# Kernel tuning notes

Measured on AMD Instinct MI355X. Metric: run time of the kernel, lower is better.

## Reference

```python
import jax, jax.numpy as jnp
import numpy as np

N = 50000      # nodes
E = 800000     # edges (avg degree 16)
SIZES = [128, 128, 128, 128, 64]
NUM_LAYERS = 4


def setup_inputs() -> dict:
    key = jax.random.key(0)
    ks = jax.random.split(key, 3 + 2 * NUM_LAYERS)
    inp = {
        "x": jax.random.normal(ks[0], (N, SIZES[0]), dtype=jnp.float32),
        "edge_index": jax.random.randint(ks[1], (2, E), 0, N, dtype=jnp.int64),
        "edge_weight": jax.random.uniform(ks[2], (E,), dtype=jnp.float32),
    }
    for i in range(NUM_LAYERS):
        fan_in = SIZES[i]
        inp[f"W{i}"] = (jax.random.normal(ks[3 + 2 * i], (SIZES[i], SIZES[i + 1]), dtype=jnp.float32)
                        / np.float32(np.sqrt(fan_in)))
        inp[f"b{i}"] = jnp.zeros((SIZES[i + 1],), dtype=jnp.float32)
    return inp


def gcn_conv(x, src, dst, ew, W, b, n):
    """PyG GCNConv with add_self_loops=True, normalize=True (eval mode).
    deg[i] = sum of incoming edge weights at i + 1 (self loop weight 1).
    norm(j->i) = deg[j]^-1/2 * w_ji * deg[i]^-1/2.
    Self loop contributes deg[i]^-1 * (xW)[i].
    """
    xw = x @ W                                                    # [n, out]
    deg = jax.ops.segment_sum(ew, dst, num_segments=n) + 1.0      # [n]
    dinv = jnp.where(deg > 0, jax.lax.rsqrt(deg), 0.0)            # deg^-1/2
    norm = dinv[src] * ew * dinv[dst]                             # [E]
    agg = jax.ops.segment_sum(xw[src] * norm[:, None], dst, num_segments=n)
    return agg + xw * (dinv * dinv)[:, None] + b


def reference(x, edge_index, edge_weight, W0, b0, W1, b1, W2, b2, W3, b3):
    # Dropout p=0.5 is identity in eval mode (training=False).
    src, dst = edge_index[0], edge_index[1]
    Ws = [W0, W1, W2, W3]
    bs = [b0, b1, b2, b3]
    for i in range(NUM_LAYERS):
        x = gcn_conv(x, src, dst, edge_weight, Ws[i], bs[i], N)
        if i < NUM_LAYERS - 1:
            x = jax.nn.relu(x)
    return x
```

## Files before the change

kernel.cpp:

```cpp
#include <hip/hip_runtime.h>
#include <hip/hip_fp16.h>


#define DEG_SCALE 4194304.0f
#define BCAP 5120
#define K1_EDGES 4096

using f16x8 = __attribute__((ext_vector_type(8))) _Float16;
using f32x4 = __attribute__((ext_vector_type(4))) float;

__global__ void prep_kernel(const float* __restrict__ W0, const float* __restrict__ W1,
                            const float* __restrict__ W2, const float* __restrict__ W3,
                            __half* P0, __half* P1, __half* P2, __half* P3,
                            int* gCursor, int nBuckets) {
    int blk = blockIdx.x;
    if (blk == 28) {
        int t = threadIdx.x;
        if (t < nBuckets) gCursor[t] = t * BCAP;
        return;
    }
    int t = blk * 256 + threadIdx.x;
    const float* W;
    __half* P;
    int OUT;
    if (t < 2048)      { W = W0; P = P0; OUT = 128; }
    else if (t < 4096) { W = W1; P = P1; OUT = 128; t -= 2048; }
    else if (t < 6144) { W = W2; P = P2; OUT = 128; t -= 4096; }
    else               { W = W3; P = P3; OUT = 64;  t -= 6144; }
    int lane = t & 63, fi = t >> 6;
    int nt = fi >> 2, kc = fi & 3;
    int col = 16 * nt + (lane & 15);
    int k0  = 32 * kc + 8 * (lane >> 4);
    union { __half h[8]; uint4 u; } v;
#pragma unroll
    for (int j = 0; j < 8; j++) v.h[j] = __float2half_rn(W[(size_t)(k0 + j) * OUT + col]);
    *(uint4*)&P[((size_t)fi * 64 + lane) * 8] = v.u;
}

__global__ __launch_bounds__(256) void bucket_scatter_kernel(
        const int* __restrict__ src, const int* __restrict__ dst,
        const float* __restrict__ ew, int* gCursor,
        int2* __restrict__ bucketArr, int E, int nBuckets) {
    __shared__ int cnt[256];
    __shared__ int runBase[256];
    int tid = threadIdx.x;
    int e0 = blockIdx.x * K1_EDGES;
    int e1 = min(e0 + K1_EDGES, E);
    cnt[tid] = 0;
    __syncthreads();
    for (int e = e0 + tid; e < e1; e += 256)
        atomicAdd(&cnt[dst[e] >> 8], 1);
    __syncthreads();
    if (tid < nBuckets && cnt[tid] > 0)
        runBase[tid] = atomicAdd(&gCursor[tid], cnt[tid]);
    __syncthreads();
    cnt[tid] = 0;
    __syncthreads();
    for (int e = e0 + tid; e < e1; e += 256) {
        int d = dst[e];
        int b = d >> 8;
        int slot = runBase[b] + atomicAdd(&cnt[b], 1);
        if (slot < (b + 1) * BCAP)
            bucketArr[slot] = make_int2((src[e] & 0xFFFF) | (d << 16),
                                        __float_as_int(ew[e]));
    }
}

__global__ __launch_bounds__(256) void bucket_csr_kernel(
        const int2* __restrict__ bucketArr, const int* __restrict__ gCursor,
        int2* __restrict__ epack, int* __restrict__ row_ptr,
        float* __restrict__ dinv, float* __restrict__ dinv2,
        int N, int E, int nBuckets) {
    __shared__ int2 st[BCAP];
    __shared__ int cnt[256];
    __shared__ int scn[256];
    __shared__ int cur[256];
    __shared__ unsigned int dfix[256];
    __shared__ int cbase_sh;
    int b   = blockIdx.x;
    int tid = threadIdx.x;
    int node0 = b << 8;
    int nloc  = min(256, N - node0);
    int base  = b * BCAP;

    int sz = (tid < nBuckets) ? (gCursor[tid] - tid * BCAP) : 0;
    scn[tid] = sz;
    __syncthreads();
    for (int off = 1; off < 256; off <<= 1) {
        int u = (tid >= off) ? scn[tid - off] : 0;
        __syncthreads();
        scn[tid] += u;
        __syncthreads();
    }
    if (tid == b) cbase_sh = scn[tid] - sz;
    cnt[tid]  = 0;
    dfix[tid] = 0u;
    __syncthreads();
    int cbase = cbase_sh;
    int size  = gCursor[b] - base;

    for (int i = tid; i < size; i += 256) {
        int2 v = bucketArr[base + i];
        st[i] = v;
        int dl = (v.x >> 16) & 255;
        atomicAdd(&cnt[dl], 1);
        atomicAdd(&dfix[dl], (unsigned int)rintf(__int_as_float(v.y) * DEG_SCALE));
    }
    __syncthreads();

    if (tid < nloc) {
        float d = (float)dfix[tid] * (1.0f / DEG_SCALE) + 1.0f;
        float r = rsqrtf(d);
        dinv[node0 + tid]  = r;
        dinv2[node0 + tid] = 1.0f / d;
    }

    int val = cnt[tid];
    scn[tid] = val;
    __syncthreads();
    for (int off = 1; off < 256; off <<= 1) {
        int u = (tid >= off) ? scn[tid - off] : 0;
        __syncthreads();
        scn[tid] += u;
        __syncthreads();
    }
    int excl = scn[tid] - val;
    scn[tid] = excl;
    if (tid < nloc) row_ptr[node0 + tid] = cbase + excl;
    if (b == nBuckets - 1 && tid == 0) row_ptr[N] = E;
    cur[tid] = 0;
    __syncthreads();

    for (int i = tid; i < size; i += 256) {
        int2 v = st[i];
        int dl = (v.x >> 16) & 255;
        int p  = cbase + scn[dl] + atomicAdd(&cur[dl], 1);
        epack[p] = v;
    }
}

template <int OUT, bool AFP32>
__device__ __forceinline__ void gemm_body(const void* __restrict__ A,
                                          const __half* __restrict__ Wpack,
                                          __half* __restrict__ xw, int nrows, int bid) {
    constexpr int NT  = OUT / 16;
    constexpr int CPR = OUT / 8;
    __shared__ __half D[64 * OUT];
    int tid  = threadIdx.x;
    int wave = tid >> 6, lane = tid & 63;
    int r = lane & 15, g = lane >> 4;
    int row0 = bid * 64 + wave * 16;

    int arow = row0 + r;
    if (arow >= nrows) arow = nrows - 1;

    f16x8 a[4];
#pragma unroll
    for (int kc = 0; kc < 4; kc++) {
        if (AFP32) {
            const float* p = (const float*)A + (size_t)arow * 128 + kc * 32 + g * 8;
            float4 u = *(const float4*)p;
            float4 v = *(const float4*)(p + 4);
            a[kc][0] = (_Float16)u.x; a[kc][1] = (_Float16)u.y;
            a[kc][2] = (_Float16)u.z; a[kc][3] = (_Float16)u.w;
            a[kc][4] = (_Float16)v.x; a[kc][5] = (_Float16)v.y;
            a[kc][6] = (_Float16)v.z; a[kc][7] = (_Float16)v.w;
        } else {
            a[kc] = *(const f16x8*)((const __half*)A + (size_t)arow * 128 + kc * 32 + g * 8);
        }
    }

#pragma unroll
    for (int nt = 0; nt < NT; nt++) {
        const f16x8* Bp = (const f16x8*)(Wpack) + (size_t)nt * 4 * 64 + lane;
        f32x4 c = {0.f, 0.f, 0.f, 0.f};
        c = __builtin_amdgcn_mfma_f32_16x16x32_f16(a[0], Bp[0],   c, 0, 0, 0);
        c = __builtin_amdgcn_mfma_f32_16x16x32_f16(a[1], Bp[64],  c, 0, 0, 0);
        c = __builtin_amdgcn_mfma_f32_16x16x32_f16(a[2], Bp[128], c, 0, 0, 0);
        c = __builtin_amdgcn_mfma_f32_16x16x32_f16(a[3], Bp[192], c, 0, 0, 0);
        int col = 16 * nt + r;
#pragma unroll
        for (int j = 0; j < 4; j++) {
            int drow = wave * 16 + 4 * g + j;
            int ch   = (col >> 3) ^ (drow & (CPR - 1));
            D[drow * OUT + ch * 8 + (col & 7)] = __float2half_rn(c[j]);
        }
    }
    __syncthreads();
#pragma unroll
    for (int i = 0; i < 64 * CPR / 256; i++) {
        int idx  = tid + i * 256;
        int drow = idx / CPR;
        int ch   = idx % CPR;
        int gr   = bid * 64 + drow;
        if (gr < nrows) {
            f16x8 v = *(f16x8*)&D[drow * OUT + ((ch ^ (drow & (CPR - 1))) << 3)];
            *(f16x8*)&xw[(size_t)gr * OUT + ch * 8] = v;
        }
    }
}

template <int OUT>
__global__ __launch_bounds__(256) void gemm_mfma_kernel(const __half* __restrict__ A,
                                                        const __half* __restrict__ Wpack,
                                                        __half* __restrict__ xw, int nrows) {
    gemm_body<OUT, false>(A, Wpack, xw, nrows, blockIdx.x);
}

__global__ __launch_bounds__(256) void norm_gemm0_kernel(
        int2* __restrict__ epack, const float* __restrict__ dinv, int E, int nbNorm,
        const float* __restrict__ x, const __half* __restrict__ Wpack,
        __half* __restrict__ xw, int nrows) {
    int blk = blockIdx.x;
    if (blk < nbNorm) {
        int i = blk * 256 + threadIdx.x;
        if (i < E) {
            int2 v = epack[i];
            int s = v.x & 0xFFFF;
            int d = (v.x >> 16) & 0xFFFF;
            float nm = dinv[s] * __int_as_float(v.y) * dinv[d];
            epack[i] = make_int2(s, __float_as_int(nm));
        }
        return;
    }
    gemm_body<128, true>(x, Wpack, xw, nrows, blk - nbNorm);
}

__global__ __launch_bounds__(256) void gather128h_kernel(const __half* __restrict__ xwh,
                                                         const int* __restrict__ rp,
                                                         const int2* __restrict__ epack,
                                                         const float* __restrict__ dinv2,
                                                         const float* __restrict__ bias,
                                                         __half* __restrict__ out, int n) {
    int lane = threadIdx.x & 63;
    int node = (blockIdx.x * blockDim.x + threadIdx.x) >> 6;
    if (node >= n) return;
    node = __builtin_amdgcn_readfirstlane(node);
    int e0 = rp[node], e1 = rp[node + 1];
    float ax = 0.f, ay = 0.f;

    int e = e0;
    for (; e + 8 <= e1; e += 8) {
        int2 v0 = epack[e + 0], v1 = epack[e + 1], v2 = epack[e + 2], v3 = epack[e + 3];
        int2 v4 = epack[e + 4], v5 = epack[e + 5], v6 = epack[e + 6], v7 = epack[e + 7];
        __half2 h0 = ((const __half2*)(xwh + (size_t)v0.x * 128))[lane];
        __half2 h1 = ((const __half2*)(xwh + (size_t)v1.x * 128))[lane];
        __half2 h2 = ((const __half2*)(xwh + (size_t)v2.x * 128))[lane];
        __half2 h3 = ((const __half2*)(xwh + (size_t)v3.x * 128))[lane];
        __half2 h4 = ((const __half2*)(xwh + (size_t)v4.x * 128))[lane];
        __half2 h5 = ((const __half2*)(xwh + (size_t)v5.x * 128))[lane];
        __half2 h6 = ((const __half2*)(xwh + (size_t)v6.x * 128))[lane];
        __half2 h7 = ((const __half2*)(xwh + (size_t)v7.x * 128))[lane];
        float w0 = __int_as_float(v0.y), w1 = __int_as_float(v1.y);
        float w2 = __int_as_float(v2.y), w3 = __int_as_float(v3.y);
        float w4 = __int_as_float(v4.y), w5 = __int_as_float(v5.y);
        float w6 = __int_as_float(v6.y), w7 = __int_as_float(v7.y);
        ax += __half2float(h0.x) * w0 + __half2float(h1.x) * w1
            + __half2float(h2.x) * w2 + __half2float(h3.x) * w3
            + __half2float(h4.x) * w4 + __half2float(h5.x) * w5
            + __half2float(h6.x) * w6 + __half2float(h7.x) * w7;
        ay += __half2float(h0.y) * w0 + __half2float(h1.y) * w1
            + __half2float(h2.y) * w2 + __half2float(h3.y) * w3
            + __half2float(h4.y) * w4 + __half2float(h5.y) * w5
            + __half2float(h6.y) * w6 + __half2float(h7.y) * w7;
    }
    for (; e + 2 <= e1; e += 2) {
        int2 v0 = epack[e + 0], v1 = epack[e + 1];
        __half2 h0 = ((const __half2*)(xwh + (size_t)v0.x * 128))[lane];
        __half2 h1 = ((const __half2*)(xwh + (size_t)v1.x * 128))[lane];
        float w0 = __int_as_float(v0.y), w1 = __int_as_float(v1.y);
        ax += __half2float(h0.x) * w0 + __half2float(h1.x) * w1;
        ay += __half2float(h0.y) * w0 + __half2float(h1.y) * w1;
    }
    for (; e < e1; e++) {
        int2 v = epack[e];
        __half2 h = ((const __half2*)(xwh + (size_t)v.x * 128))[lane];
        float w = __int_as_float(v.y);
        ax += __half2float(h.x) * w;
        ay += __half2float(h.y) * w;
    }

    float   d2 = dinv2[node];
    __half2 hs = ((const __half2*)(xwh + (size_t)node * 128))[lane];
    float2  bl = *(const float2*)&bias[lane * 2];
    float ox = fmaxf(ax + __half2float(hs.x) * d2 + bl.x, 0.f);
    float oy = fmaxf(ay + __half2float(hs.y) * d2 + bl.y, 0.f);
    __half2 ho;
    ho.x = __float2half_rn(ox);
    ho.y = __float2half_rn(oy);
    *(__half2*)&out[(size_t)node * 128 + lane * 2] = ho;
}

__global__ __launch_bounds__(256) void gather64h_kernel(const __half* __restrict__ xwh,
                                                        const int* __restrict__ rp,
                                                        const int2* __restrict__ epack,
                                                        const float* __restrict__ dinv2,
                                                        const float* __restrict__ bias,
                                                        float* __restrict__ out, int n) {
    int lane = threadIdx.x & 63;
    int node = (blockIdx.x * blockDim.x + threadIdx.x) >> 6;
    if (node >= n) return;
    node = __builtin_amdgcn_readfirstlane(node);
    int e0 = rp[node], e1 = rp[node + 1];
    float acc = 0.f;

    int e = e0;
    for (; e + 8 <= e1; e += 8) {
        int2 v0 = epack[e + 0], v1 = epack[e + 1], v2 = epack[e + 2], v3 = epack[e + 3];
        int2 v4 = epack[e + 4], v5 = epack[e + 5], v6 = epack[e + 6], v7 = epack[e + 7];
        float r0 = __half2float(xwh[(size_t)v0.x * 64 + lane]);
        float r1 = __half2float(xwh[(size_t)v1.x * 64 + lane]);
        float r2 = __half2float(xwh[(size_t)v2.x * 64 + lane]);
        float r3 = __half2float(xwh[(size_t)v3.x * 64 + lane]);
        float r4 = __half2float(xwh[(size_t)v4.x * 64 + lane]);
        float r5 = __half2float(xwh[(size_t)v5.x * 64 + lane]);
        float r6 = __half2float(xwh[(size_t)v6.x * 64 + lane]);
        float r7 = __half2float(xwh[(size_t)v7.x * 64 + lane]);
        acc += r0 * __int_as_float(v0.y) + r1 * __int_as_float(v1.y)
             + r2 * __int_as_float(v2.y) + r3 * __int_as_float(v3.y)
             + r4 * __int_as_float(v4.y) + r5 * __int_as_float(v5.y)
             + r6 * __int_as_float(v6.y) + r7 * __int_as_float(v7.y);
    }
    for (; e < e1; e++) {
        int2 v = epack[e];
        acc += __half2float(xwh[(size_t)v.x * 64 + lane]) * __int_as_float(v.y);
    }

    float self = __half2float(xwh[(size_t)node * 64 + lane]);
    out[(size_t)node * 64 + lane] = acc + self * dinv2[node] + bias[lane];
}

extern "C" void kernel_launch(void* const* d_in, const int* in_sizes, int n_in,
                              void* d_out, int out_size, void* d_ws, size_t ws_size,
                              hipStream_t stream) {
    const float* x  = (const float*)d_in[0];
    const int*   ei = (const int*)d_in[1];
    const float* ew = (const float*)d_in[2];
    const float* W[4] = {(const float*)d_in[3], (const float*)d_in[5],
                         (const float*)d_in[7], (const float*)d_in[9]};
    const float* b[4] = {(const float*)d_in[4], (const float*)d_in[6],
                         (const float*)d_in[8], (const float*)d_in[10]};
    const int N = in_sizes[0] / 128;
    const int E = in_sizes[2];
    const int* srcIdx = ei;
    const int* dstIdx = ei + E;
    float* out = (float*)d_out;

    const int nBuckets = (N + 255) / 256;

    char* p = (char*)d_ws;
    auto alloc = [&](size_t bytes) -> char* {
        char* q = p;
        p += (bytes + 255) / 256 * 256;
        return q;
    };
    float*  dinv      = (float*)alloc((size_t)N * 4);
    float*  dinv2     = (float*)alloc((size_t)N * 4);
    int*    row_ptr   = (int*)alloc((size_t)(N + 1) * 4);
    int*    gCursor   = (int*)alloc(256 * 4);
    int2*   bucketArr = (int2*)alloc((size_t)nBuckets * BCAP * 8);
    int2*   epack     = (int2*)alloc((size_t)E * 8);
    __half* xwh       = (__half*)alloc((size_t)N * 128 * 2);
    __half* bufA      = (__half*)alloc((size_t)N * 128 * 2);
    __half* Wp[4];
    Wp[0] = (__half*)alloc(128 * 128 * 2);
    Wp[1] = (__half*)alloc(128 * 128 * 2);
    Wp[2] = (__half*)alloc(128 * 128 * 2);
    Wp[3] = (__half*)alloc(128 * 64 * 2);

    const int k1_grid = (E + K1_EDGES - 1) / K1_EDGES;
    const int eb      = (E + 255) / 256;
    const int gemm_grid   = (N + 63) / 64;
    const int gather_grid = (N + 3) / 4;

    prep_kernel<<<29, 256, 0, stream>>>(W[0], W[1], W[2], W[3],
                                        Wp[0], Wp[1], Wp[2], Wp[3],
                                        gCursor, nBuckets);
    bucket_scatter_kernel<<<k1_grid, 256, 0, stream>>>(srcIdx, dstIdx, ew, gCursor,
                                                       bucketArr, E, nBuckets);
    bucket_csr_kernel<<<nBuckets, 256, 0, stream>>>(bucketArr, gCursor, epack,
                                                    row_ptr, dinv, dinv2, N, E, nBuckets);
    norm_gemm0_kernel<<<eb + gemm_grid, 256, 0, stream>>>(epack, dinv, E, eb,
                                                          x, Wp[0], xwh, N);

    const __half* xin;
    for (int i = 0; i < 4; i++) {
        if (i < 3) {
            if (i > 0)
                gemm_mfma_kernel<128><<<gemm_grid, 256, 0, stream>>>(xin, Wp[i], xwh, N);
            gather128h_kernel<<<gather_grid, 256, 0, stream>>>(
                xwh, row_ptr, epack, dinv2, b[i], bufA, N);
            xin = bufA;
        } else {
            gemm_mfma_kernel<64><<<gemm_grid, 256, 0, stream>>>(xin, Wp[3], xwh, N);
            gather64h_kernel<<<gather_grid, 256, 0, stream>>>(
                xwh, row_ptr, epack, dinv2, b[3], out, N);
        }
    }
}
```

Before: 210.5 us.

## Fuse layer gather with next layer's MFMA GEMM in one kernel

Replaces the separate gather128h and gemm_mfma kernels for the hidden layers with one kernel. Each block gathers and aggregates 16 nodes into shared memory, applies bias and ReLU, then multiplies that tile by the next layer's weights with MFMA and writes xW directly. The intent is to remove the round trip of the activation buffer through global memory and three kernel launches. In exchange, each block holds 16 nodes instead of 64, so weights are reloaded more often and the GEMM tile is smaller.

Result: faster. 182.7 us (-13.2%).

```diff
diff --git a/kernel.cpp b/kernel.cpp
--- a/kernel.cpp
+++ b/kernel.cpp
@@ -5,6 +5,7 @@
 #define DEG_SCALE 4194304.0f
 #define BCAP 5120
 #define K1_EDGES 4096
+#define ACT_LD 136
 
 using f16x8 = __attribute__((ext_vector_type(8))) _Float16;
 using f32x4 = __attribute__((ext_vector_type(4))) float;
@@ -200,13 +201,6 @@
     }
 }
 
-template <int OUT>
-__global__ __launch_bounds__(256) void gemm_mfma_kernel(const __half* __restrict__ A,
-                                                        const __half* __restrict__ Wpack,
-                                                        __half* __restrict__ xw, int nrows) {
-    gemm_body<OUT, false>(A, Wpack, xw, nrows, blockIdx.x);
-}
-
 __global__ __launch_bounds__(256) void norm_gemm0_kernel(
         int2* __restrict__ epack, const float* __restrict__ dinv, int E, int nbNorm,
         const float* __restrict__ x, const __half* __restrict__ Wpack,
@@ -226,69 +220,121 @@
     gemm_body<128, true>(x, Wpack, xw, nrows, blk - nbNorm);
 }
 
-__global__ __launch_bounds__(256) void gather128h_kernel(const __half* __restrict__ xwh,
-                                                         const int* __restrict__ rp,
-                                                         const int2* __restrict__ epack,
-                                                         const float* __restrict__ dinv2,
-                                                         const float* __restrict__ bias,
-                                                         __half* __restrict__ out, int n) {
-    int lane = threadIdx.x & 63;
-    int node = (blockIdx.x * blockDim.x + threadIdx.x) >> 6;
-    if (node >= n) return;
-    node = __builtin_amdgcn_readfirstlane(node);
-    int e0 = rp[node], e1 = rp[node + 1];
-    float ax = 0.f, ay = 0.f;
-
-    int e = e0;
-    for (; e + 8 <= e1; e += 8) {
-        int2 v0 = epack[e + 0], v1 = epack[e + 1], v2 = epack[e + 2], v3 = epack[e + 3];
-        int2 v4 = epack[e + 4], v5 = epack[e + 5], v6 = epack[e + 6], v7 = epack[e + 7];
-        __half2 h0 = ((const __half2*)(xwh + (size_t)v0.x * 128))[lane];
-        __half2 h1 = ((const __half2*)(xwh + (size_t)v1.x * 128))[lane];
-        __half2 h2 = ((const __half2*)(xwh + (size_t)v2.x * 128))[lane];
-        __half2 h3 = ((const __half2*)(xwh + (size_t)v3.x * 128))[lane];
-        __half2 h4 = ((const __half2*)(xwh + (size_t)v4.x * 128))[lane];
-        __half2 h5 = ((const __half2*)(xwh + (size_t)v5.x * 128))[lane];
-        __half2 h6 = ((const __half2*)(xwh + (size_t)v6.x * 128))[lane];
-        __half2 h7 = ((const __half2*)(xwh + (size_t)v7.x * 128))[lane];
-        float w0 = __int_as_float(v0.y), w1 = __int_as_float(v1.y);
-        float w2 = __int_as_float(v2.y), w3 = __int_as_float(v3.y);
-        float w4 = __int_as_float(v4.y), w5 = __int_as_float(v5.y);
-        float w6 = __int_as_float(v6.y), w7 = __int_as_float(v7.y);
-        ax += __half2float(h0.x) * w0 + __half2float(h1.x) * w1
-            + __half2float(h2.x) * w2 + __half2float(h3.x) * w3
-            + __half2float(h4.x) * w4 + __half2float(h5.x) * w5
-            + __half2float(h6.x) * w6 + __half2float(h7.x) * w7;
-        ay += __half2float(h0.y) * w0 + __half2float(h1.y) * w1
-            + __half2float(h2.y) * w2 + __half2float(h3.y) * w3
-            + __half2float(h4.y) * w4 + __half2float(h5.y) * w5
-            + __half2float(h6.y) * w6 + __half2float(h7.y) * w7;
-    }
-    for (; e + 2 <= e1; e += 2) {
-        int2 v0 = epack[e + 0], v1 = epack[e + 1];
-        __half2 h0 = ((const __half2*)(xwh + (size_t)v0.x * 128))[lane];
-        __half2 h1 = ((const __half2*)(xwh + (size_t)v1.x * 128))[lane];
-        float w0 = __int_as_float(v0.y), w1 = __int_as_float(v1.y);
-        ax += __half2float(h0.x) * w0 + __half2float(h1.x) * w1;
-        ay += __half2float(h0.y) * w0 + __half2float(h1.y) * w1;
-    }
-    for (; e < e1; e++) {
-        int2 v = epack[e];
-        __half2 h = ((const __half2*)(xwh + (size_t)v.x * 128))[lane];
-        float w = __int_as_float(v.y);
-        ax += __half2float(h.x) * w;
-        ay += __half2float(h.y) * w;
-    }
-
-    float   d2 = dinv2[node];
-    __half2 hs = ((const __half2*)(xwh + (size_t)node * 128))[lane];
-    float2  bl = *(const float2*)&bias[lane * 2];
-    float ox = fmaxf(ax + __half2float(hs.x) * d2 + bl.x, 0.f);
-    float oy = fmaxf(ay + __half2float(hs.y) * d2 + bl.y, 0.f);
-    __half2 ho;
-    ho.x = __float2half_rn(ox);
-    ho.y = __float2half_rn(oy);
-    *(__half2*)&out[(size_t)node * 128 + lane * 2] = ho;
+template <int OUT_NEXT>
+__global__ __launch_bounds__(256) void gather_gemm_kernel(
+        const __half* __restrict__ xwh,
+        const int* __restrict__ rp,
+        const int2* __restrict__ epack,
+        const float* __restrict__ dinv2,
+        const float* __restrict__ bias,
+        const __half* __restrict__ Wpack,
+        __half* __restrict__ xw_out,
+        int n) {
+    constexpr int NT  = OUT_NEXT / 16;
+    constexpr int NTW = NT / 4;
+    constexpr int CPR = OUT_NEXT / 8;
+    __shared__ __half act[16 * ACT_LD];
+    __shared__ __half D[16 * OUT_NEXT];
+    int tid  = threadIdx.x;
+    int wv   = tid >> 6, lane = tid & 63;
+    int node0 = blockIdx.x * 16;
+
+#pragma unroll
+    for (int k = 0; k < 4; k++) {
+        int lrow = wv * 4 + k;
+        int node = node0 + lrow;
+        if (node < n) {
+            node = __builtin_amdgcn_readfirstlane(node);
+            int e0 = rp[node], e1 = rp[node + 1];
+            float ax = 0.f, ay = 0.f;
+            int e = e0;
+            for (; e + 8 <= e1; e += 8) {
+                int2 v0 = epack[e + 0], v1 = epack[e + 1], v2 = epack[e + 2], v3 = epack[e + 3];
+                int2 v4 = epack[e + 4], v5 = epack[e + 5], v6 = epack[e + 6], v7 = epack[e + 7];
+                __half2 h0 = ((const __half2*)(xwh + (size_t)v0.x * 128))[lane];
+                __half2 h1 = ((const __half2*)(xwh + (size_t)v1.x * 128))[lane];
+                __half2 h2 = ((const __half2*)(xwh + (size_t)v2.x * 128))[lane];
+                __half2 h3 = ((const __half2*)(xwh + (size_t)v3.x * 128))[lane];
+                __half2 h4 = ((const __half2*)(xwh + (size_t)v4.x * 128))[lane];
+                __half2 h5 = ((const __half2*)(xwh + (size_t)v5.x * 128))[lane];
+                __half2 h6 = ((const __half2*)(xwh + (size_t)v6.x * 128))[lane];
+                __half2 h7 = ((const __half2*)(xwh + (size_t)v7.x * 128))[lane];
+                float w0 = __int_as_float(v0.y), w1 = __int_as_float(v1.y);
+                float w2 = __int_as_float(v2.y), w3 = __int_as_float(v3.y);
+                float w4 = __int_as_float(v4.y), w5 = __int_as_float(v5.y);
+                float w6 = __int_as_float(v6.y), w7 = __int_as_float(v7.y);
+                ax += __half2float(h0.x) * w0 + __half2float(h1.x) * w1
+                    + __half2float(h2.x) * w2 + __half2float(h3.x) * w3
+                    + __half2float(h4.x) * w4 + __half2float(h5.x) * w5
+                    + __half2float(h6.x) * w6 + __half2float(h7.x) * w7;
+                ay += __half2float(h0.y) * w0 + __half2float(h1.y) * w1
+                    + __half2float(h2.y) * w2 + __half2float(h3.y) * w3
+                    + __half2float(h4.y) * w4 + __half2float(h5.y) * w5
+                    + __half2float(h6.y) * w6 + __half2float(h7.y) * w7;
+            }
+            for (; e + 2 <= e1; e += 2) {
+                int2 v0 = epack[e + 0], v1 = epack[e + 1];
+                __half2 h0 = ((const __half2*)(xwh + (size_t)v0.x * 128))[lane];
+                __half2 h1 = ((const __half2*)(xwh + (size_t)v1.x * 128))[lane];
+                float w0 = __int_as_float(v0.y), w1 = __int_as_float(v1.y);
+                ax += __half2float(h0.x) * w0 + __half2float(h1.x) * w1;
+                ay += __half2float(h0.y) * w0 + __half2float(h1.y) * w1;
+            }
+            for (; e < e1; e++) {
+                int2 v = epack[e];
+                __half2 h = ((const __half2*)(xwh + (size_t)v.x * 128))[lane];
+                float w = __int_as_float(v.y);
+                ax += __half2float(h.x) * w;
+                ay += __half2float(h.y) * w;
+            }
+            float   d2 = dinv2[node];
+            __half2 hs = ((const __half2*)(xwh + (size_t)node * 128))[lane];
+            float2  bl = *(const float2*)&bias[lane * 2];
+            float ox = fmaxf(ax + __half2float(hs.x) * d2 + bl.x, 0.f);
+            float oy = fmaxf(ay + __half2float(hs.y) * d2 + bl.y, 0.f);
+            __half2 ho;
+            ho.x = __float2half_rn(ox);
+            ho.y = __float2half_rn(oy);
+            *(__half2*)&act[lrow * ACT_LD + lane * 2] = ho;
+        }
+    }
+    __syncthreads();
+
+    int r = lane & 15, g = lane >> 4;
+    f16x8 a[4];
+#pragma unroll
+    for (int kc = 0; kc < 4; kc++)
+        a[kc] = *(const f16x8*)&act[r * ACT_LD + kc * 32 + g * 8];
+
+#pragma unroll
+    for (int t = 0; t < NTW; t++) {
+        int nt = wv * NTW + t;
+        const f16x8* Bp = (const f16x8*)(Wpack) + (size_t)nt * 4 * 64 + lane;
+        f32x4 c = {0.f, 0.f, 0.f, 0.f};
+        c = __builtin_amdgcn_mfma_f32_16x16x32_f16(a[0], Bp[0],   c, 0, 0, 0);
+        c = __builtin_amdgcn_mfma_f32_16x16x32_f16(a[1], Bp[64],  c, 0, 0, 0);
+        c = __builtin_amdgcn_mfma_f32_16x16x32_f16(a[2], Bp[128], c, 0, 0, 0);
+        c = __builtin_amdgcn_mfma_f32_16x16x32_f16(a[3], Bp[192], c, 0, 0, 0);
+        int col = 16 * nt + r;
+#pragma unroll
+        for (int j = 0; j < 4; j++) {
+            int drow = 4 * g + j;
+            int ch   = (col >> 3) ^ (drow & (CPR - 1));
+            D[drow * OUT_NEXT + ch * 8 + (col & 7)] = __float2half_rn(c[j]);
+        }
+    }
+    __syncthreads();
+
+    constexpr int CHUNKS = 16 * CPR;
+    if (tid < CHUNKS) {
+        int drow = tid / CPR;
+        int ch   = tid % CPR;
+        int gr   = node0 + drow;
+        if (gr < n) {
+            f16x8 v = *(f16x8*)&D[drow * OUT_NEXT + ((ch ^ (drow & (CPR - 1))) << 3)];
+            *(f16x8*)&xw_out[(size_t)gr * OUT_NEXT + ch * 8] = v;
+        }
+    }
 }
 
 __global__ __launch_bounds__(256) void gather64h_kernel(const __half* __restrict__ xwh,
@@ -360,8 +406,8 @@
     int*    gCursor   = (int*)alloc(256 * 4);
     int2*   bucketArr = (int2*)alloc((size_t)nBuckets * BCAP * 8);
     int2*   epack     = (int2*)alloc((size_t)E * 8);
-    __half* xwh       = (__half*)alloc((size_t)N * 128 * 2);
-    __half* bufA      = (__half*)alloc((size_t)N * 128 * 2);
+    __half* xwA       = (__half*)alloc((size_t)N * 128 * 2);
+    __half* xwB       = (__half*)alloc((size_t)N * 128 * 2);
     __half* Wp[4];
     Wp[0] = (__half*)alloc(128 * 128 * 2);
     Wp[1] = (__half*)alloc(128 * 128 * 2);
@@ -370,8 +416,9 @@
 
     const int k1_grid = (E + K1_EDGES - 1) / K1_EDGES;
     const int eb      = (E + 255) / 256;
-    const int gemm_grid   = (N + 63) / 64;
-    const int gather_grid = (N + 3) / 4;
+    const int gemm_grid  = (N + 63) / 64;
+    const int fused_grid = (N + 15) / 16;
+    const int g64_grid   = (N + 3) / 4;
 
     prep_kernel<<<29, 256, 0, stream>>>(W[0], W[1], W[2], W[3],
                                         Wp[0], Wp[1], Wp[2], Wp[3],
@@ -381,20 +428,13 @@
     bucket_csr_kernel<<<nBuckets, 256, 0, stream>>>(bucketArr, gCursor, epack,
                                                     row_ptr, dinv, dinv2, N, E, nBuckets);
     norm_gemm0_kernel<<<eb + gemm_grid, 256, 0, stream>>>(epack, dinv, E, eb,
-                                                          x, Wp[0], xwh, N);
-
-    const __half* xin;
-    for (int i = 0; i < 4; i++) {
-        if (i < 3) {
-            if (i > 0)
-                gemm_mfma_kernel<128><<<gemm_grid, 256, 0, stream>>>(xin, Wp[i], xwh, N);
-            gather128h_kernel<<<gather_grid, 256, 0, stream>>>(
-                xwh, row_ptr, epack, dinv2, b[i], bufA, N);
-            xin = bufA;
-        } else {
-            gemm_mfma_kernel<64><<<gemm_grid, 256, 0, stream>>>(xin, Wp[3], xwh, N);
-            gather64h_kernel<<<gather_grid, 256, 0, stream>>>(
-                xwh, row_ptr, epack, dinv2, b[3], out, N);
-        }
-    }
-}
+                                                          x, Wp[0], xwA, N);
+    gather_gemm_kernel<128><<<fused_grid, 256, 0, stream>>>(
+        xwA, row_ptr, epack, dinv2, b[0], Wp[1], xwB, N);
+    gather_gemm_kernel<128><<<fused_grid, 256, 0, stream>>>(
+        xwB, row_ptr, epack, dinv2, b[1], Wp[2], xwA, N);
+    gather_gemm_kernel<64><<<fused_grid, 256, 0, stream>>>(
+        xwA, row_ptr, epack, dinv2, b[2], Wp[3], xwB, N);
+    gather64h_kernel<<<g64_grid, 256, 0, stream>>>(
+        xwB, row_ptr, epack, dinv2, b[3], out, N);
+}
```
